# Kernel tuning notes

Measured on AMD Instinct MI355X. Metric: run time of the kernel, lower is better.

The kernel has to match this reference:

```python
import jax, jax.numpy as jnp
import numpy as np

N_VERT = 40962  # icosphere level-6 vertex count
K = 7           # 1-ring neighborhood size (self + 6 neighbors)


def setup_inputs() -> dict:
    key = jax.random.key(0)
    k1, k2, k3 = jax.random.split(key, 3)
    x = jax.random.normal(k1, (16, 256, N_VERT), dtype=jnp.float32)
    neigh_orders = jax.random.randint(k2, (N_VERT * K,), 0, N_VERT, dtype=jnp.int32)
    W = jax.random.normal(k3, (1, 2 * K), dtype=jnp.float32) * 0.1  # Linear(14 -> 1) weight
    b = jnp.zeros((1,), dtype=jnp.float32)
    return {"x": x, "neigh_orders": neigh_orders, "W": W, "b": b}


def reference(x, neigh_orders, W, b):
    # x: [B, C, N] features on spherical mesh vertices
    avg = jnp.mean(x, axis=1, keepdims=True)          # [B, 1, N] (AdaptiveAvgPool2d((1,None)))
    mx = jnp.max(x, axis=1, keepdims=True)            # [B, 1, N] (AdaptiveMaxPool2d((1,None)))
    pool = jnp.concatenate([avg, mx], axis=1)         # [B, 2, N]
    p = jnp.transpose(pool, (0, 2, 1))                # [B, N, 2]
    idx = neigh_orders.reshape(N_VERT, K)             # [N, 7] 1-ring neighbor indices
    g = p[:, idx, :]                                  # [B, N, 7, 2] neighbor gather
    g = g.reshape(p.shape[0], N_VERT, 2 * K)          # [B, N, 14]
    out = jnp.einsum('bnf,of->bno', g, W) + b         # [B, N, 1] Linear(14 -> 1)
    att = jax.nn.sigmoid(out)
    return jnp.transpose(att, (0, 2, 1))              # [B, 1, N] spatial attention map
```

## Files before the change

kernel.cpp:

```cpp
#include <hip/hip_runtime.h>
#include <math.h>

#define B_DIM 16
#define C_DIM 256
#define NV    40962
#define K_NEI 7
#define NPAIR (NV / 2)
#define GRP   10241

typedef float v2f __attribute__((ext_vector_type(2)));

__global__ __launch_bounds__(256) void pool_kernel(const float* __restrict__ x,
                                                   float4* __restrict__ pool) {
    int t = blockIdx.x * 256 + threadIdx.x;
    if (t >= B_DIM * GRP) return;
    int b = t / GRP;
    int r = t - b * GRP;
    int n0 = 4 * r; if (n0 > NV - 4) n0 = NV - 4;

    const float* xb = x + (size_t)b * C_DIM * NV + n0;

    float s0 = 0.f, s1 = 0.f, s2 = 0.f, s3 = 0.f;
    float m0 = -INFINITY, m1 = -INFINITY, m2 = -INFINITY, m3 = -INFINITY;
    #pragma unroll 16
    for (int c = 0; c < C_DIM; ++c) {
        const float* p = xb + (size_t)c * NV;
        v2f va = __builtin_nontemporal_load(reinterpret_cast<const v2f*>(p));
        v2f vb = __builtin_nontemporal_load(reinterpret_cast<const v2f*>(p + 2));
        s0 += va.x; s1 += va.y; s2 += vb.x; s3 += vb.y;
        m0 = fmaxf(m0, va.x); m1 = fmaxf(m1, va.y);
        m2 = fmaxf(m2, vb.x); m3 = fmaxf(m3, vb.y);
    }
    const float inv = 1.0f / (float)C_DIM;
    size_t f4 = ((size_t)b * NV + n0) >> 1;
    pool[f4]     = make_float4(s0 * inv, m0, s1 * inv, m1);
    pool[f4 + 1] = make_float4(s2 * inv, m2, s3 * inv, m3);
}

__global__ void transpose_kernel(const float2* __restrict__ pool,
                                 float2* __restrict__ poolT) {
    __shared__ float2 tile[64][17];
    int n0 = blockIdx.x * 64;
    int i  = threadIdx.x & 63;
    int bq = threadIdx.x >> 6;
    #pragma unroll
    for (int p = 0; p < 4; ++p) {
        int b = p * 4 + bq;
        if (n0 + i < NV)
            tile[i][b] = pool[(size_t)b * NV + n0 + i];
    }
    __syncthreads();
    int valid = NV - n0; if (valid > 64) valid = 64;
    int nf4 = valid * 8;
    float4* dst = reinterpret_cast<float4*>(poolT + (size_t)n0 * 16);
    for (int e = threadIdx.x; e < nf4; e += 256) {
        int e2 = e * 2;
        int n  = e2 >> 4;
        int b  = e2 & 15;
        float2 a0 = tile[n][b];
        float2 a1 = tile[n][b + 1];
        dst[e] = make_float4(a0.x, a0.y, a1.x, a1.y);
    }
}

__global__ void att4_kernel(const float2* __restrict__ poolT,
                            const int* __restrict__ idx,
                            const float* __restrict__ W,
                            const float* __restrict__ bias,
                            float* __restrict__ out) {
    int tid = threadIdx.x;
    int n   = blockIdx.x * 64 + (tid >> 2);
    int bq  = tid & 3;
    if (n >= NV) return;

    float w[2 * K_NEI];
    #pragma unroll
    for (int i = 0; i < 2 * K_NEI; ++i) w[i] = W[i];
    float bb = bias[0];

    float acc[4];
    #pragma unroll
    for (int r = 0; r < 4; ++r) acc[r] = bb;

    #pragma unroll
    for (int k = 0; k < K_NEI; ++k) {
        int j = idx[n * K_NEI + k];
        const float4* L = reinterpret_cast<const float4*>(poolT + (size_t)j * 16 + bq * 4);
        float4 v0 = L[0];
        float4 v1 = L[1];
        acc[0] = fmaf(w[2 * k + 1], v0.y, fmaf(w[2 * k], v0.x, acc[0]));
        acc[1] = fmaf(w[2 * k + 1], v0.w, fmaf(w[2 * k], v0.z, acc[1]));
        acc[2] = fmaf(w[2 * k + 1], v1.y, fmaf(w[2 * k], v1.x, acc[2]));
        acc[3] = fmaf(w[2 * k + 1], v1.w, fmaf(w[2 * k], v1.z, acc[3]));
    }
    #pragma unroll
    for (int r = 0; r < 4; ++r)
        out[(size_t)(bq * 4 + r) * NV + n] = 1.0f / (1.0f + expf(-acc[r]));
}

extern "C" void kernel_launch(void* const* d_in, const int* in_sizes, int n_in,
                              void* d_out, int out_size, void* d_ws, size_t ws_size,
                              hipStream_t stream) {
    const float* x     = (const float*)d_in[0];
    const int*   neigh = (const int*)  d_in[1];
    const float* W     = (const float*)d_in[2];
    const float* bias  = (const float*)d_in[3];
    float*       out   = (float*)d_out;

    const size_t POOL_BYTES = (size_t)B_DIM * NV * sizeof(float2);

    float4* pool4 = (float4*)d_ws;
    float2* poolT = (float2*)((char*)d_ws + POOL_BYTES);

    int t1 = B_DIM * GRP;
    pool_kernel<<<(t1 + 255) / 256, 256, 0, stream>>>(x, pool4);

    int ntile = (NV + 63) / 64;
    transpose_kernel<<<ntile, 256, 0, stream>>>((const float2*)d_ws, poolT);
    att4_kernel<<<ntile, 256, 0, stream>>>(poolT, neigh, W, bias, out);
}
```

Baseline: 128.8 us.

## Fuse pool, transpose and attention kernels into one persistent kernel with grid barriers

```diff
diff --git a/kernel.cpp b/kernel.cpp
--- a/kernel.cpp
+++ b/kernel.cpp
@@ -5,97 +5,114 @@
 #define C_DIM 256
 #define NV    40962
 #define K_NEI 7
-#define NPAIR (NV / 2)
 #define GRP   10241
+#define NBLK  641
 
 typedef float v2f __attribute__((ext_vector_type(2)));
 
-__global__ __launch_bounds__(256) void pool_kernel(const float* __restrict__ x,
-                                                   float4* __restrict__ pool) {
-    int t = blockIdx.x * 256 + threadIdx.x;
-    if (t >= B_DIM * GRP) return;
-    int b = t / GRP;
-    int r = t - b * GRP;
-    int n0 = 4 * r; if (n0 > NV - 4) n0 = NV - 4;
-
-    const float* xb = x + (size_t)b * C_DIM * NV + n0;
-
-    float s0 = 0.f, s1 = 0.f, s2 = 0.f, s3 = 0.f;
-    float m0 = -INFINITY, m1 = -INFINITY, m2 = -INFINITY, m3 = -INFINITY;
-    #pragma unroll 16
-    for (int c = 0; c < C_DIM; ++c) {
-        const float* p = xb + (size_t)c * NV;
-        v2f va = __builtin_nontemporal_load(reinterpret_cast<const v2f*>(p));
-        v2f vb = __builtin_nontemporal_load(reinterpret_cast<const v2f*>(p + 2));
-        s0 += va.x; s1 += va.y; s2 += vb.x; s3 += vb.y;
-        m0 = fmaxf(m0, va.x); m1 = fmaxf(m1, va.y);
-        m2 = fmaxf(m2, vb.x); m3 = fmaxf(m3, vb.y);
+__device__ __forceinline__ void grid_barrier(unsigned* cnt) {
+    __syncthreads();
+    if (threadIdx.x == 0) {
+        __threadfence();
+        atomicAdd(cnt, 1u);
+        while (__hip_atomic_load(cnt, __ATOMIC_RELAXED,
+                                 __HIP_MEMORY_SCOPE_AGENT) < NBLK) {
+            __builtin_amdgcn_s_sleep(1);
+        }
+        __threadfence();
     }
-    const float inv = 1.0f / (float)C_DIM;
-    size_t f4 = ((size_t)b * NV + n0) >> 1;
-    pool[f4]     = make_float4(s0 * inv, m0, s1 * inv, m1);
-    pool[f4 + 1] = make_float4(s2 * inv, m2, s3 * inv, m3);
+    __syncthreads();
 }
 
-__global__ void transpose_kernel(const float2* __restrict__ pool,
-                                 float2* __restrict__ poolT) {
-    __shared__ float2 tile[64][17];
-    int n0 = blockIdx.x * 64;
-    int i  = threadIdx.x & 63;
-    int bq = threadIdx.x >> 6;
-    #pragma unroll
-    for (int p = 0; p < 4; ++p) {
-        int b = p * 4 + bq;
-        if (n0 + i < NV)
-            tile[i][b] = pool[(size_t)b * NV + n0 + i];
+__global__ __launch_bounds__(256, 3)
+void fused_kernel(const float* __restrict__ x, const int* __restrict__ idx,
+                  const float* __restrict__ W, const float* __restrict__ bias,
+                  float* __restrict__ out,
+                  float2* pool, float2* poolT, unsigned* bar) {
+    {
+        int t = blockIdx.x * 256 + threadIdx.x;
+        if (t < B_DIM * GRP) {
+            int b = t / GRP;
+            int r = t - b * GRP;
+            int n0 = 4 * r; if (n0 > NV - 4) n0 = NV - 4;
+
+            const float* xb = x + (size_t)b * C_DIM * NV + n0;
+            float s0 = 0.f, s1 = 0.f, s2 = 0.f, s3 = 0.f;
+            float m0 = -INFINITY, m1 = -INFINITY, m2 = -INFINITY, m3 = -INFINITY;
+            #pragma unroll 16
+            for (int c = 0; c < C_DIM; ++c) {
+                const float* p = xb + (size_t)c * NV;
+                v2f va = __builtin_nontemporal_load(reinterpret_cast<const v2f*>(p));
+                v2f vb = __builtin_nontemporal_load(reinterpret_cast<const v2f*>(p + 2));
+                s0 += va.x; s1 += va.y; s2 += vb.x; s3 += vb.y;
+                m0 = fmaxf(m0, va.x); m1 = fmaxf(m1, va.y);
+                m2 = fmaxf(m2, vb.x); m3 = fmaxf(m3, vb.y);
+            }
+            const float inv = 1.0f / (float)C_DIM;
+            float4* pool4 = reinterpret_cast<float4*>(pool);
+            size_t f4 = ((size_t)b * NV + n0) >> 1;
+            pool4[f4]     = make_float4(s0 * inv, m0, s1 * inv, m1);
+            pool4[f4 + 1] = make_float4(s2 * inv, m2, s3 * inv, m3);
+        }
     }
-    __syncthreads();
-    int valid = NV - n0; if (valid > 64) valid = 64;
-    int nf4 = valid * 8;
-    float4* dst = reinterpret_cast<float4*>(poolT + (size_t)n0 * 16);
-    for (int e = threadIdx.x; e < nf4; e += 256) {
-        int e2 = e * 2;
-        int n  = e2 >> 4;
-        int b  = e2 & 15;
-        float2 a0 = tile[n][b];
-        float2 a1 = tile[n][b + 1];
-        dst[e] = make_float4(a0.x, a0.y, a1.x, a1.y);
+    grid_barrier(bar + 0);
+
+    {
+        __shared__ float2 tile[64][17];
+        int n0 = blockIdx.x * 64;
+        int i  = threadIdx.x & 63;
+        int bq = threadIdx.x >> 6;
+        #pragma unroll
+        for (int p = 0; p < 4; ++p) {
+            int b = p * 4 + bq;
+            if (n0 + i < NV)
+                tile[i][b] = pool[(size_t)b * NV + n0 + i];
+        }
+        __syncthreads();
+        int valid = NV - n0; if (valid > 64) valid = 64;
+        int nf4 = valid * 8;
+        float4* dst = reinterpret_cast<float4*>(poolT + (size_t)n0 * 16);
+        for (int e = threadIdx.x; e < nf4; e += 256) {
+            int e2 = e * 2;
+            int n  = e2 >> 4;
+            int b  = e2 & 15;
+            float2 a0 = tile[n][b];
+            float2 a1 = tile[n][b + 1];
+            dst[e] = make_float4(a0.x, a0.y, a1.x, a1.y);
+        }
     }
-}
+    grid_barrier(bar + 1);
 
-__global__ void att4_kernel(const float2* __restrict__ poolT,
-                            const int* __restrict__ idx,
-                            const float* __restrict__ W,
-                            const float* __restrict__ bias,
-                            float* __restrict__ out) {
-    int tid = threadIdx.x;
-    int n   = blockIdx.x * 64 + (tid >> 2);
-    int bq  = tid & 3;
-    if (n >= NV) return;
+    {
+        int tid = threadIdx.x;
+        int n   = blockIdx.x * 64 + (tid >> 2);
+        int bq  = tid & 3;
+        if (n < NV) {
+            float w[2 * K_NEI];
+            #pragma unroll
+            for (int i = 0; i < 2 * K_NEI; ++i) w[i] = W[i];
+            float bb = bias[0];
 
-    float w[2 * K_NEI];
-    #pragma unroll
-    for (int i = 0; i < 2 * K_NEI; ++i) w[i] = W[i];
-    float bb = bias[0];
+            float acc[4];
+            #pragma unroll
+            for (int r = 0; r < 4; ++r) acc[r] = bb;
 
-    float acc[4];
-    #pragma unroll
-    for (int r = 0; r < 4; ++r) acc[r] = bb;
-
-    #pragma unroll
-    for (int k = 0; k < K_NEI; ++k) {
-        int j = idx[n * K_NEI + k];
-        const float4* L = reinterpret_cast<const float4*>(poolT + (size_t)j * 16 + bq * 4);
-        float4 v0 = L[0];
-        float4 v1 = L[1];
-        acc[0] = fmaf(w[2 * k + 1], v0.y, fmaf(w[2 * k], v0.x, acc[0]));
-        acc[1] = fmaf(w[2 * k + 1], v0.w, fmaf(w[2 * k], v0.z, acc[1]));
-        acc[2] = fmaf(w[2 * k + 1], v1.y, fmaf(w[2 * k], v1.x, acc[2]));
-        acc[3] = fmaf(w[2 * k + 1], v1.w, fmaf(w[2 * k], v1.z, acc[3]));
+            #pragma unroll
+            for (int k = 0; k < K_NEI; ++k) {
+                int j = idx[n * K_NEI + k];
+                const float4* L = reinterpret_cast<const float4*>(poolT + (size_t)j * 16 + bq * 4);
+                float4 v0 = L[0];
+                float4 v1 = L[1];
+                acc[0] = fmaf(w[2 * k + 1], v0.y, fmaf(w[2 * k], v0.x, acc[0]));
+                acc[1] = fmaf(w[2 * k + 1], v0.w, fmaf(w[2 * k], v0.z, acc[1]));
+                acc[2] = fmaf(w[2 * k + 1], v1.y, fmaf(w[2 * k], v1.x, acc[2]));
+                acc[3] = fmaf(w[2 * k + 1], v1.w, fmaf(w[2 * k], v1.z, acc[3]));
+            }
+            #pragma unroll
+            for (int r = 0; r < 4; ++r)
+                out[(size_t)(bq * 4 + r) * NV + n] = 1.0f / (1.0f + expf(-acc[r]));
+        }
     }
-    #pragma unroll
-    for (int r = 0; r < 4; ++r)
-        out[(size_t)(bq * 4 + r) * NV + n] = 1.0f / (1.0f + expf(-acc[r]));
 }
 
 extern "C" void kernel_launch(void* const* d_in, const int* in_sizes, int n_in,
@@ -109,13 +126,11 @@
 
     const size_t POOL_BYTES = (size_t)B_DIM * NV * sizeof(float2);
 
-    float4* pool4 = (float4*)d_ws;
-    float2* poolT = (float2*)((char*)d_ws + POOL_BYTES);
+    float2*   pool  = (float2*)d_ws;
+    float2*   poolT = (float2*)((char*)d_ws + POOL_BYTES);
+    unsigned* bar   = (unsigned*)((char*)d_ws + 2 * POOL_BYTES);
 
-    int t1 = B_DIM * GRP;
-    pool_kernel<<<(t1 + 255) / 256, 256, 0, stream>>>(x, pool4);
+    hipMemsetAsync(bar, 0, 2 * sizeof(unsigned), stream);
 
-    int ntile = (NV + 63) / 64;
-    transpose_kernel<<<ntile, 256, 0, stream>>>((const float2*)d_ws, poolT);
-    att4_kernel<<<ntile, 256, 0, stream>>>(poolT, neigh, W, bias, out);
+    fused_kernel<<<NBLK, 256, 0, stream>>>(x, neigh, W, bias, out, pool, poolT, bar);
 }
```

New measurement: 280.8 us. 2.18x slower.
